# Kernel tuning notes

Measured on AMD Instinct MI355X. Metric: run time of the kernel, lower is better.

The kernel has to match this reference:

```python
import jax, jax.numpy as jnp
import numpy as np

N_NODES = 20000
N_EDGES = 320000
N_GRAPHS = 200
N_LAYERS = 2
TOWERS = 5
F_IN = 75        # divide_input=False -> each tower sees the full 75-dim input
F_OUT = 15       # out_channels // towers = 75 // 5
EDGE_DIM = 50
POST_IN = (4 * 3 + 1) * F_IN  # 4 aggregators * 3 scalers + self = 975
EPS_STD = 1e-5
EPS_BN = 1e-5


def setup_inputs() -> dict:
    key = jax.random.key(0)
    ks = jax.random.split(key, 16)
    x_idx = jax.random.randint(ks[0], (N_NODES,), 0, 10000)
    edge_index = jax.random.randint(ks[1], (2, N_EDGES), 0, N_NODES)
    edge_attr_idx = jax.random.randint(ks[2], (N_EDGES,), 0, 100)
    batch_idx = jnp.sort(jax.random.randint(ks[3], (N_NODES,), 0, N_GRAPHS))

    def g(k, shp, fan):
        return jax.random.normal(k, shp, jnp.float32) * np.float32(1.0 / np.sqrt(fan))

    inp = dict(
        x_idx=x_idx, edge_index=edge_index, edge_attr_idx=edge_attr_idx, batch_idx=batch_idx,
        node_emb=g(ks[4], (10000, F_IN), 1.0),
        edge_emb=g(ks[5], (100, EDGE_DIM), 1.0),
        W_edge=g(ks[6], (N_LAYERS, EDGE_DIM, F_IN), EDGE_DIM),
        b_edge=jnp.zeros((N_LAYERS, F_IN), jnp.float32),
        W_pre=g(ks[7], (N_LAYERS, TOWERS, 3 * F_IN, F_IN), 3 * F_IN),
        b_pre=jnp.zeros((N_LAYERS, TOWERS, F_IN), jnp.float32),
        W_post=g(ks[8], (N_LAYERS, TOWERS, POST_IN, F_OUT), POST_IN),
        b_post=jnp.zeros((N_LAYERS, TOWERS, F_OUT), jnp.float32),
        W_lin=g(ks[9], (N_LAYERS, F_IN, F_IN), F_IN),
        b_lin=jnp.zeros((N_LAYERS, F_IN), jnp.float32),
        bn_gamma=jnp.ones((N_LAYERS, F_IN), jnp.float32),
        bn_beta=jnp.zeros((N_LAYERS, F_IN), jnp.float32),
        W1=g(ks[10], (75, 50), 75), b1=jnp.zeros((50,), jnp.float32),
        W2=g(ks[11], (50, 25), 50), b2=jnp.zeros((25,), jnp.float32),
        W3=g(ks[12], (25, 1), 25), b3=jnp.zeros((1,), jnp.float32),
    )
    return inp


def reference(x_idx, edge_index, edge_attr_idx, batch_idx,
              node_emb, edge_emb, W_edge, b_edge, W_pre, b_pre,
              W_post, b_post, W_lin, b_lin, bn_gamma, bn_beta,
              W1, b1, W2, b2, W3, b3):
    src, dst = edge_index[0], edge_index[1]  # flow source_to_target: aggregate at dst
    x = node_emb[x_idx]                      # [N, 75]
    e_raw = edge_emb[edge_attr_idx]          # [E, 50]

    # in-degree based scalers (PNA); avg log-degree from this graph's degree histogram
    deg = jax.ops.segment_sum(jnp.ones((N_EDGES,), jnp.float32), dst, num_segments=N_NODES)
    avg_log = jnp.mean(jnp.log(deg + 1.0))
    deg_c = jnp.maximum(deg, 1.0)
    amp = (jnp.log(deg_c + 1.0) / avg_log)[:, None, None]
    att = (avg_log / jnp.log(deg_c + 1.0))[:, None, None]
    has_in = (deg > 0.0)[:, None, None]
    inv_deg = (1.0 / deg_c)[:, None, None]

    for l in range(N_LAYERS):
        # edge encoder (shared across towers)
        e = e_raw @ W_edge[l] + b_edge[l]                            # [E, 75]
        # message: since divide_input=False all towers see the same concat input
        h = jnp.concatenate([x[dst], x[src], e], axis=-1)            # [E, 225]
        m = jnp.einsum('ec,tcf->etf', h, W_pre[l]) + b_pre[l]        # [E, T, 75]
        # multi-aggregator reduction at dst
        mean = jax.ops.segment_sum(m, dst, num_segments=N_NODES) * inv_deg
        mean_sq = jax.ops.segment_sum(m * m, dst, num_segments=N_NODES) * inv_deg
        std = jnp.sqrt(jax.nn.relu(mean_sq - mean * mean) + EPS_STD)
        mn = jnp.where(has_in, jax.ops.segment_min(m, dst, num_segments=N_NODES), 0.0)
        mx = jnp.where(has_in, jax.ops.segment_max(m, dst, num_segments=N_NODES), 0.0)
        aggr = jnp.concatenate([mean, mn, mx, std], axis=-1)         # [N, T, 300]
        # degree scalers: identity, amplification, attenuation
        out = jnp.concatenate([aggr, aggr * amp, aggr * att], axis=-1)  # [N, T, 900]
        # update: concat self features, per-tower post MLP, then shared lin
        xt = jnp.broadcast_to(x[:, None, :], (N_NODES, TOWERS, F_IN))
        h2 = jnp.concatenate([xt, out], axis=-1)                     # [N, T, 975]
        y = jnp.einsum('ntc,tcf->ntf', h2, W_post[l]) + b_post[l]    # [N, T, 15]
        y = y.reshape(N_NODES, TOWERS * F_OUT) @ W_lin[l] + b_lin[l] # [N, 75]
        # BatchNorm (training-mode batch stats, biased variance) + ReLU
        mu = jnp.mean(y, axis=0)
        var = jnp.mean((y - mu) ** 2, axis=0)
        y = (y - mu) * jax.lax.rsqrt(var + EPS_BN) * bn_gamma[l] + bn_beta[l]
        x = jax.nn.relu(y)

    pooled = jax.ops.segment_sum(x, batch_idx, num_segments=N_GRAPHS)  # [G, 75]
    h = jax.nn.relu(pooled @ W1 + b1)
    h = jax.nn.relu(h @ W2 + b2)
    return h @ W3 + b3                                               # [G, 1]
```

## Files before the change

kernel.cpp:

```cpp
#include <hip/hip_runtime.h>
#include <hip/hip_bf16.h>
#include <math.h>

#define NN 20000
#define NE 320000
#define NG 200
#define FI 75
#define NT 5
#define FO 15
#define CH 375
#define PI 975

typedef __attribute__((ext_vector_type(8))) short v8s;
typedef __attribute__((ext_vector_type(4))) float v4f;

__device__ __forceinline__ unsigned short f2bfu(float v) {
  __hip_bfloat16 h = __float2bfloat16(v);
  return *reinterpret_cast<unsigned short*>(&h);
}
__device__ __forceinline__ float uif(unsigned u) { return __uint_as_float(u); }

__global__ __launch_bounds__(256) void k_mega1(
    const int* __restrict__ xidx, const float* __restrict__ emb, float* __restrict__ x,
    const int* __restrict__ dstp, int* __restrict__ deg,
    const float* __restrict__ eemb, const float* __restrict__ W_edge,
    const float* __restrict__ b_edge, float* __restrict__ te,
    const float* __restrict__ W_pre, float* __restrict__ WAs,
    const float* __restrict__ W_post, float* __restrict__ V,
    const float* __restrict__ b_post, const float* __restrict__ W_lin,
    const float* __restrict__ b_lin, float* __restrict__ bc) {
  __shared__ float S[FI * 16];
  int b = blockIdx.x, tid = threadIdx.x;
  if (b < 5860) {
    int i = b * 256 + tid;
    if (i < NN * FI) {
      int n = i / FI, f = i - n * FI;
      x[i] = emb[xidx[n] * FI + f];
    }
  } else if (b < 7110) {
    int e = (b - 5860) * 256 + tid;
    if (e < NE) atomicAdd(&deg[dstp[e]], 1);
  } else if (b < 7310) {
    int la = b - 7110;
    int l = la / 100, a = la - l * 100;
    int f = tid;
    if (f < FI) {
      float acc = b_edge[l * FI + f];
      for (int j = 0; j < 50; ++j)
        acc = fmaf(eemb[a * 50 + j], W_edge[(l * 50 + j) * FI + f], acc);
      te[la * FI + f] = acc;
    }
  } else if (b < 7530) {
    int i = (b - 7310) * 256 + tid;
    if (i < 2 * FI * CH) {
      int c = i % CH;
      int k = (i / CH) % FI;
      int l = i / (CH * FI);
      int t = c / FI, f = c - t * FI;
      WAs[i] = W_pre[((size_t)(l * NT + t) * 225 + FI + k) * FI + f];
    }
  } else if (b < 7560) {
    int bid = b - 7530;
    int g = bid % 3;
    int lt = bid / 3;
    for (int idx = tid; idx < FI * 16; idx += 256) {
      int q = idx >> 4, f = idx & 15;
      float v = 0.f;
      if (f < FO) {
        const float* wb = W_post + (size_t)lt * PI * FO;
        int rowb = FI + g * 300 + q;
        v = wb[rowb * FO + f] + wb[(rowb + FI) * FO + f] + wb[(rowb + 2 * FI) * FO + f];
      }
      S[idx] = v;
    }
    __syncthreads();
    for (int idx = tid; idx < FI * 16; idx += 256) {
      int j = idx >> 4, f = idx & 15;
      float acc = 0.f;
      const float* wr = W_pre + ((size_t)lt * 225 + j) * FI;
      for (int q = 0; q < FI; ++q) acc = fmaf(wr[q], S[q * 16 + f], acc);
      V[((size_t)bid * FI + j) * 16 + f] = acc;
    }
  } else {
    int l = b - 7560;
    int g = tid;
    if (g < FI) {
      float acc = b_lin[l * FI + g];
      for (int j = 0; j < FI; ++j)
        acc = fmaf(b_post[l * FI + j], W_lin[(l * FI + j) * FI + g], acc);
      bc[l * 76 + g] = acc;
    }
  }
}

__global__ __launch_bounds__(1024) void k_mega2(
    const int* __restrict__ deg, int* __restrict__ off, int* __restrict__ cur,
    float* __restrict__ avglog,
    const float* __restrict__ te, const float* __restrict__ W_pre,
    const float* __restrict__ b_pre, unsigned short* __restrict__ tm,
    const float* __restrict__ W_post, const float* __restrict__ V,
    unsigned short* __restrict__ Bp,
    const float* __restrict__ WAs, unsigned short* __restrict__ Bxs) {
  __shared__ float red[1024];
  int b = blockIdx.x, t = threadIdx.x;
  if (b == 0) {
    int* wsum = (int*)red;
    int base = t * 20;
    int loc[20];
    int s = 0;
#pragma unroll
    for (int j = 0; j < 20; ++j) {
      int i = base + j;
      int v = (i < NN) ? deg[i] : 0;
      loc[j] = s;
      s += v;
    }
    int lane = t & 63, w = t >> 6;
    int inc = s;
    for (int o = 1; o < 64; o <<= 1) {
      int u = __shfl_up(inc, o, 64);
      if (lane >= o) inc += u;
    }
    if (lane == 63) wsum[w] = inc;
    __syncthreads();
    if (t == 0) {
      int a = 0;
#pragma unroll
      for (int k = 0; k < 16; ++k) { int v = wsum[k]; wsum[k] = a; a += v; }
    }
    __syncthreads();
    int tex = wsum[w] + inc - s;
#pragma unroll
    for (int j = 0; j < 20; ++j) {
      int i = base + j;
      if (i < NN) { int e = tex + loc[j]; off[i] = e; cur[i] = e; }
    }
    if (t == 1023) off[NN] = tex + s;
  } else if (b == 1) {
    float s = 0.f;
    for (int i = t; i < NN; i += 1024) s += logf((float)deg[i] + 1.f);
    red[t] = s;
    __syncthreads();
    for (int o = 512; o > 0; o >>= 1) {
      if (t < o) red[t] += red[t + o];
      __syncthreads();
    }
    if (t == 0) avglog[0] = red[0] / (float)NN;
  } else if (b < 77) {
    int idx = (b - 2) * 1024 + t;
    if (idx < 76800) {
      int la = idx / 384, c = idx - la * 384;
      int l = la / 100;
      float acc = 0.f;
      if (c < CH) {
        int tt = c / FI, f = c - tt * FI;
        acc = b_pre[(l * NT + tt) * FI + f];
        const float* ter = te + la * FI;
        for (int k = 0; k < FI; ++k)
          acc = fmaf(ter[k], W_pre[((size_t)(l * NT + tt) * 225 + 150 + k) * FI + f], acc);
      }
      tm[(size_t)la * 384 + c] = f2bfu(acc);
    }
  } else if (b < 302) {
    int i = (b - 77) * 1024 + t;
    if (i < 230400) {
      int j = i & 7;
      int lane = (i >> 3) & 63;
      int rem = i >> 9;
      int kb = rem % 15; rem /= 15;
      int g = rem % 3; rem /= 3;
      int tt = rem % 5;
      int l = rem / 5;
      int k = kb * 32 + (lane >> 4) * 8 + j;
      int f = lane & 15;
      float w = 0.f;
      if (f < FO) {
        int lt = l * NT + tt;
        if (k < 300) {
          int a = k / 75, ch = k - a * 75;
          w = W_post[((size_t)lt * PI + FI + g * 300 + a * 75 + ch) * FO + f];
        } else if (k >= 320 && k < 395) {
          w = V[(((size_t)(lt * 3 + g)) * FI + (k - 320)) * 16 + f];
        } else if (k >= 395 && k < 470 && g == 0) {
          w = W_post[((size_t)lt * PI + (k - 395)) * FO + f];
        }
      }
      Bp[i] = f2bfu(w);
    }
  } else {
    int i = (b - 302) * 1024 + t;
    if (i < 73728) {
      int j = i & 7;
      int lane = (i >> 3) & 63;
      int rem = i >> 9;
      int nt = rem % 24; rem /= 24;
      int kb = rem % 3;
      int l = rem / 3;
      int k = kb * 32 + (lane >> 4) * 8 + j;
      int n = nt * 16 + (lane & 15);
      float w = 0.f;
      if (k < FI && n < CH) w = WAs[(size_t)l * FI * CH + k * CH + n];
      Bxs[i] = f2bfu(w);
    }
  }
}

__global__ __launch_bounds__(256) void k_mega3(
    const int* __restrict__ srcp, const int* __restrict__ dstp,
    const int* __restrict__ attr, int* __restrict__ cur, int2* __restrict__ csr,
    const int* __restrict__ deg, const float* __restrict__ avglog,
    float* __restrict__ amp, float* __restrict__ att, float* __restrict__ inv) {
  int b = blockIdx.x, t = threadIdx.x;
  if (b < 1250) {
    int e = b * 256 + t;
    if (e < NE) {
      int pos = atomicAdd(&cur[dstp[e]], 1);
      csr[pos] = make_int2(srcp[e], attr[e]);
    }
  } else {
    int i = (b - 1250) * 256 + t;
    if (i < NN) {
      float dc = fmaxf((float)deg[i], 1.f);
      float ld = logf(dc + 1.f);
      float av = avglog[0];
      amp[i] = ld / av;
      att[i] = av / ld;
      inv[i] = 1.f / dc;
    }
  }
}

__global__ __launch_bounds__(256) void k_gemm_xs(const float* __restrict__ x,
                                                 const unsigned short* __restrict__ BxsL,
                                                 unsigned short* __restrict__ xsb,
                                                 const int* __restrict__ deg,
                                                 unsigned short* __restrict__ xh,
                                                 float* __restrict__ bnsum) {
  int tid = threadIdx.x;
  if (blockIdx.y == 1) {
    if (blockIdx.x == 0 && tid < 150) bnsum[tid] = 0.f;
    for (int i = blockIdx.x * 256 + tid; i < NN * 160; i += 625 * 256) {
      int r = i / 160, k = i - r * 160;
      float v = 0.f;
      if (k < FI) v = x[(size_t)r * FI + k] * ((deg[r] > 0) ? 1.f : 0.f);
      else if (k < 150) v = x[(size_t)r * FI + k - FI];
      xh[i] = f2bfu(v);
    }
    return;
  }
  __shared__ unsigned short As[32 * 104];
  __shared__ unsigned short Os[32 * 384];
  int m0 = blockIdx.x * 32;
  for (int i = tid; i < 32 * 104; i += 256) {
    int r = i / 104, k = i - r * 104;
    As[i] = (k < FI) ? f2bfu(x[(size_t)(m0 + r) * FI + k]) : 0;
  }
  __syncthreads();
  int lane = tid & 63, w = tid >> 6;
  int m16 = lane & 15, quad = lane >> 4;
  v4f acc0[6], acc1[6];
#pragma unroll
  for (int nt = 0; nt < 6; ++nt) {
    acc0[nt] = {0.f, 0.f, 0.f, 0.f};
    acc1[nt] = {0.f, 0.f, 0.f, 0.f};
  }
  const unsigned short* arow0 = As + m16 * 104 + quad * 8;
  const unsigned short* arow1 = As + (16 + m16) * 104 + quad * 8;
#pragma unroll
  for (int kb = 0; kb < 3; ++kb) {
    v8s a0 = *(const v8s*)(arow0 + kb * 32);
    v8s a1 = *(const v8s*)(arow1 + kb * 32);
#pragma unroll
    for (int nt = 0; nt < 6; ++nt) {
      v8s bf = *(const v8s*)(BxsL + ((size_t)(kb * 24 + w * 6 + nt) * 64 + lane) * 8);
      acc0[nt] = __builtin_amdgcn_mfma_f32_16x16x32_bf16(a0, bf, acc0[nt], 0, 0, 0);
      acc1[nt] = __builtin_amdgcn_mfma_f32_16x16x32_bf16(a1, bf, acc1[nt], 0, 0, 0);
    }
  }
#pragma unroll
  for (int nt = 0; nt < 6; ++nt) {
    int col = w * 96 + nt * 16 + m16;
#pragma unroll
    for (int r = 0; r < 4; ++r) {
      Os[(quad * 4 + r) * 384 + col] = f2bfu(acc0[nt][r]);
      Os[(16 + quad * 4 + r) * 384 + col] = f2bfu(acc1[nt][r]);
    }
  }
  __syncthreads();
  uint4* dst = (uint4*)(xsb + (size_t)m0 * 384);
  const uint4* src = (const uint4*)Os;
  for (int i = tid; i < 1536; i += 256) dst[i] = src[i];
}

__global__ __launch_bounds__(192) void k_aggregate(int n0, int cn,
    const unsigned short* __restrict__ xs, const int2* __restrict__ csr,
    const int* __restrict__ off, const float* __restrict__ inv_deg,
    const unsigned short* __restrict__ tm, unsigned short* __restrict__ aggA) {
  __shared__ unsigned short sm[4 * 1600];
  int tid = threadIdx.x;
  int sub = tid / 48;
  int lane48 = tid - sub * 48;
  int rel0 = blockIdx.x * 4;
  int rel = rel0 + sub;
  for (int idx = tid; idx < 400; idx += 192) {
    int h = idx / 100, pp = idx - h * 100;
    int t = pp / 20, cc = pp - t * 20;
    sm[h * 1600 + t * 320 + 300 + cc] = 0;
  }
  if (rel < cn) {
    int n = n0 + rel;
    int c0 = lane48 * 8;
    int o0 = off[n], o1 = off[n + 1];
    float s[8], q[8], mn[8], mx[8];
#pragma unroll
    for (int j = 0; j < 8; ++j) {
      s[j] = 0.f; q[j] = 0.f; mn[j] = INFINITY; mx[j] = -INFINITY;
    }
    auto proc = [&](uint4 xv, uint4 tv) {
      unsigned xa[4] = {xv.x, xv.y, xv.z, xv.w};
      unsigned ta[4] = {tv.x, tv.y, tv.z, tv.w};
#pragma unroll
      for (int j = 0; j < 4; ++j) {
        float z0 = uif(xa[j] << 16) + uif(ta[j] << 16);
        float z1 = uif(xa[j] & 0xffff0000u) + uif(ta[j] & 0xffff0000u);
        s[2 * j] += z0; q[2 * j] = fmaf(z0, z0, q[2 * j]);
        mn[2 * j] = fminf(mn[2 * j], z0); mx[2 * j] = fmaxf(mx[2 * j], z0);
        s[2 * j + 1] += z1; q[2 * j + 1] = fmaf(z1, z1, q[2 * j + 1]);
        mn[2 * j + 1] = fminf(mn[2 * j + 1], z1); mx[2 * j + 1] = fmaxf(mx[2 * j + 1], z1);
      }
    };
    int i = o0;
    for (; i + 8 <= o1; i += 8) {
      int2 e0 = csr[i], e1 = csr[i + 1], e2 = csr[i + 2], e3 = csr[i + 3];
      int2 e4 = csr[i + 4], e5 = csr[i + 5], e6 = csr[i + 6], e7 = csr[i + 7];
      uint4 x0 = *(const uint4*)(xs + (size_t)e0.x * 384 + c0);
      uint4 t0 = *(const uint4*)(tm + (size_t)e0.y * 384 + c0);
      uint4 x1 = *(const uint4*)(xs + (size_t)e1.x * 384 + c0);
      uint4 t1 = *(const uint4*)(tm + (size_t)e1.y * 384 + c0);
      uint4 x2 = *(const uint4*)(xs + (size_t)e2.x * 384 + c0);
      uint4 t2 = *(const uint4*)(tm + (size_t)e2.y * 384 + c0);
      uint4 x3 = *(const uint4*)(xs + (size_t)e3.x * 384 + c0);
      uint4 t3 = *(const uint4*)(tm + (size_t)e3.y * 384 + c0);
      uint4 x4 = *(const uint4*)(xs + (size_t)e4.x * 384 + c0);
      uint4 t4 = *(const uint4*)(tm + (size_t)e4.y * 384 + c0);
      uint4 x5 = *(const uint4*)(xs + (size_t)e5.x * 384 + c0);
      uint4 t5 = *(const uint4*)(tm + (size_t)e5.y * 384 + c0);
      uint4 x6 = *(const uint4*)(xs + (size_t)e6.x * 384 + c0);
      uint4 t6 = *(const uint4*)(tm + (size_t)e6.y * 384 + c0);
      uint4 x7 = *(const uint4*)(xs + (size_t)e7.x * 384 + c0);
      uint4 t7 = *(const uint4*)(tm + (size_t)e7.y * 384 + c0);
      proc(x0, t0); proc(x1, t1); proc(x2, t2); proc(x3, t3);
      proc(x4, t4); proc(x5, t5); proc(x6, t6); proc(x7, t7);
    }
    for (; i + 2 <= o1; i += 2) {
      int2 e0 = csr[i], e1 = csr[i + 1];
      uint4 x0 = *(const uint4*)(xs + (size_t)e0.x * 384 + c0);
      uint4 t0 = *(const uint4*)(tm + (size_t)e0.y * 384 + c0);
      uint4 x1 = *(const uint4*)(xs + (size_t)e1.x * 384 + c0);
      uint4 t1 = *(const uint4*)(tm + (size_t)e1.y * 384 + c0);
      proc(x0, t0); proc(x1, t1);
    }
    if (i < o1) {
      int2 e0 = csr[i];
      uint4 x0 = *(const uint4*)(xs + (size_t)e0.x * 384 + c0);
      uint4 t0 = *(const uint4*)(tm + (size_t)e0.y * 384 + c0);
      proc(x0, t0);
    }
    float inv = inv_deg[n];
    bool empty = (o1 == o0);
    unsigned short* srow = sm + sub * 1600;
#pragma unroll
    for (int j = 0; j < 8; ++j) {
      int c = c0 + j;
      if (c < CH) {
        float me = s[j] * inv;
        float sd = sqrtf(fmaxf(q[j] * inv - me * me, 0.f) + 1e-5f);
        float mnv = empty ? 0.f : mn[j];
        float mxv = empty ? 0.f : mx[j];
        int t = c / 75, ch = c - t * 75;
        unsigned short* bb = srow + t * 320;
        bb[ch] = f2bfu(me);
        bb[75 + ch] = f2bfu(mnv);
        bb[150 + ch] = f2bfu(mxv);
        bb[225 + ch] = f2bfu(sd);
      }
    }
  }
  __syncthreads();
  int nrow = cn - rel0;
  if (nrow > 4) nrow = 4;
  if (nrow > 0) {
    int nu4 = nrow * 200;
    uint4* dst = (uint4*)(aggA + (size_t)rel0 * 1600);
    const uint4* src = (const uint4*)sm;
    for (int idx = tid; idx < nu4; idx += 192) dst[idx] = src[idx];
  }
}

__global__ __launch_bounds__(128) void k_post2(int n0, int nend,
    const unsigned short* __restrict__ aggA, const unsigned short* __restrict__ xh,
    const unsigned short* __restrict__ Bp, const float* __restrict__ amp,
    const float* __restrict__ att, const float* __restrict__ Wl,
    const float* __restrict__ bcL, float* __restrict__ yout,
    float* __restrict__ bnsum) {
  __shared__ float zs[32][76];
  __shared__ float Ws[FI * 76];
  __shared__ float ysum[FI], ysq[FI];
  int tid = threadIdx.x;
  for (int i = tid; i < FI * FI; i += 128) {
    int k = i / FI, f = i - k * FI;
    Ws[k * 76 + f] = Wl[i];
  }
  if (tid < FI) { ysum[tid] = 0.f; ysq[tid] = 0.f; }
  int lane = tid & 63, wv = tid >> 6;
  int m16 = lane & 15, quad = lane >> 4;
  int relA = blockIdx.x * 32 + wv * 16 + m16;
  const unsigned short* arow = aggA + (size_t)relA * 1600 + quad * 8;
  const unsigned short* xrow = xh + (size_t)(n0 + relA) * 160 + quad * 8;
  for (int t = 0; t < NT; ++t) {
    const unsigned short* bp = Bp + ((size_t)t * 3 * 15 * 64) * 8 + lane * 8;
    v4f a0 = {0.f, 0.f, 0.f, 0.f}, a1 = a0, a2 = a0;
#pragma unroll
    for (int kb = 0; kb < 15; ++kb) {
      v8s av = *(const v8s*)((kb < 10) ? (arow + t * 320 + kb * 32)
                                       : (xrow + (kb - 10) * 32));
      const unsigned short* bb = bp + (size_t)kb * 512;
      v8s b0 = *(const v8s*)(bb);
      v8s b1 = *(const v8s*)(bb + 15 * 512);
      v8s b2 = *(const v8s*)(bb + 30 * 512);
      a0 = __builtin_amdgcn_mfma_f32_16x16x32_bf16(av, b0, a0, 0, 0, 0);
      a1 = __builtin_amdgcn_mfma_f32_16x16x32_bf16(av, b1, a1, 0, 0, 0);
      a2 = __builtin_amdgcn_mfma_f32_16x16x32_bf16(av, b2, a2, 0, 0, 0);
    }
    int f = m16;
    if (f < FO) {
      int relD0 = wv * 16 + quad * 4;
#pragma unroll
      for (int r = 0; r < 4; ++r) {
        int nd = n0 + blockIdx.x * 32 + relD0 + r;
        if (nd < nend) {
          float zz = a0[r] + amp[nd] * a1[r] + att[nd] * a2[r];
          zs[relD0 + r][t * FO + f] = zz;
        }
      }
    }
  }
  __syncthreads();
  int nl = tid >> 2, fg = tid & 3;
  int f0 = fg * 19;
  int n = n0 + blockIdx.x * 32 + nl;
  if (n < nend) {
    float acc[19];
#pragma unroll
    for (int i = 0; i < 19; ++i) acc[i] = bcL[f0 + i];
    for (int k = 0; k < FI; ++k) {
      float a = zs[nl][k];
#pragma unroll
      for (int i = 0; i < 19; ++i) acc[i] = fmaf(a, Ws[k * 76 + f0 + i], acc[i]);
    }
#pragma unroll
    for (int i = 0; i < 19; ++i) {
      int f = f0 + i;
      if (f < FI) {
        float v = acc[i];
        yout[(size_t)n * FI + f] = v;
        atomicAdd(&ysum[f], v);
        atomicAdd(&ysq[f], v * v);
      }
    }
  }
  __syncthreads();
  if (tid < FI) {
    atomicAdd(&bnsum[tid], ysum[tid]);
    atomicAdd(&bnsum[FI + tid], ysq[tid]);
  }
}

__global__ __launch_bounds__(256) void k_bnfinapply(const float* __restrict__ y,
    const float* __restrict__ bnsum, const float* __restrict__ gamL,
    const float* __restrict__ betL, float* __restrict__ xo,
    const int* __restrict__ batch, float* __restrict__ pooled, int dopool) {
  __shared__ float sc[150];
  int tid = threadIdx.x;
  if (tid < FI) {
    float mu = bnsum[tid] / (float)NN;
    float var = bnsum[FI + tid] / (float)NN - mu * mu;
    float scl = gamL[tid] * rsqrtf(var + 1e-5f);
    sc[tid] = scl;
    sc[FI + tid] = betL[tid] - mu * scl;
  }
  if (!dopool) {
    for (int i = blockIdx.x * 256 + tid; i < NG * FI; i += gridDim.x * 256)
      pooled[i] = 0.f;
  }
  __syncthreads();
  int stride = gridDim.x * 256;
  for (int i = blockIdx.x * 256 + tid; i < NN * FI; i += stride) {
    int n = i / FI, f = i - n * FI;
    float v = fmaxf(fmaf(y[i], sc[f], sc[FI + f]), 0.f);
    xo[i] = v;
    if (dopool) atomicAdd(&pooled[batch[n] * FI + f], v);
  }
}

__global__ void k_head(const float* __restrict__ pooled, const float* __restrict__ W1,
                       const float* __restrict__ b1, const float* __restrict__ W2,
                       const float* __restrict__ b2, const float* __restrict__ W3,
                       const float* __restrict__ b3, float* __restrict__ out) {
  __shared__ float p[FI], h1[50], h2[25];
  int g = blockIdx.x, t = threadIdx.x;
  for (int i = t; i < FI; i += 64) p[i] = pooled[g * FI + i];
  __syncthreads();
  if (t < 50) {
    float a = b1[t];
    for (int j = 0; j < FI; ++j) a = fmaf(p[j], W1[j * 50 + t], a);
    h1[t] = fmaxf(a, 0.f);
  }
  __syncthreads();
  if (t < 25) {
    float a = b2[t];
    for (int j = 0; j < 50; ++j) a = fmaf(h1[j], W2[j * 25 + t], a);
    h2[t] = fmaxf(a, 0.f);
  }
  __syncthreads();
  if (t == 0) {
    float a = b3[0];
    for (int j = 0; j < 25; ++j) a = fmaf(h2[j], W3[j], a);
    out[g] = a;
  }
}

extern "C" void kernel_launch(void* const* d_in, const int* in_sizes, int n_in,
                              void* d_out, int out_size, void* d_ws, size_t ws_size,
                              hipStream_t stream) {
  const int* x_idx = (const int*)d_in[0];
  const int* eidx  = (const int*)d_in[1];
  const int* srcp  = eidx;
  const int* dstp  = eidx + NE;
  const int* eattr = (const int*)d_in[2];
  const int* batch = (const int*)d_in[3];
  const float* node_emb = (const float*)d_in[4];
  const float* edge_emb = (const float*)d_in[5];
  const float* W_edge = (const float*)d_in[6];
  const float* b_edge = (const float*)d_in[7];
  const float* W_pre  = (const float*)d_in[8];
  const float* b_pre  = (const float*)d_in[9];
  const float* W_post = (const float*)d_in[10];
  const float* b_post = (const float*)d_in[11];
  const float* W_lin  = (const float*)d_in[12];
  const float* b_lin  = (const float*)d_in[13];
  const float* gam = (const float*)d_in[14];
  const float* bet = (const float*)d_in[15];
  const float* W1 = (const float*)d_in[16];
  const float* b1 = (const float*)d_in[17];
  const float* W2 = (const float*)d_in[18];
  const float* b2 = (const float*)d_in[19];
  const float* W3 = (const float*)d_in[20];
  const float* b3 = (const float*)d_in[21];

  char* p = (char*)d_ws;
  auto alloc = [&](size_t b) -> char* {
    char* r = p;
    p += (b + 255) & ~(size_t)255;
    return r;
  };
  float* x_a   = (float*)alloc((size_t)NN * FI * 4);
  float* x_b   = (float*)alloc((size_t)NN * FI * 4);
  unsigned short* xs_bf = (unsigned short*)alloc((size_t)NN * 384 * 2);
  float* z     = (float*)alloc((size_t)NN * FI * 4);
  unsigned short* xh = (unsigned short*)alloc((size_t)(NN + 32) * 160 * 2);
  float* te    = (float*)alloc(2 * 100 * FI * 4);
  unsigned short* tm_bf = (unsigned short*)alloc((size_t)2 * 100 * 384 * 2);
  float* WAs   = (float*)alloc((size_t)2 * FI * CH * 4);
  float* V     = (float*)alloc((size_t)2 * NT * 3 * FI * 16 * 4);
  unsigned short* Bpk = (unsigned short*)alloc((size_t)230400 * 2);
  unsigned short* Bxs = (unsigned short*)alloc((size_t)73728 * 2);
  float* bc    = (float*)alloc(2 * 76 * 4);
  float* ampv  = (float*)alloc((size_t)NN * 4);
  float* attv  = (float*)alloc((size_t)NN * 4);
  float* invv  = (float*)alloc((size_t)NN * 4);
  float* avglog = (float*)alloc(256);
  float* bnsum = (float*)alloc(2 * FI * 4);
  float* pooled = (float*)alloc((size_t)NG * FI * 4);
  int* deg = (int*)alloc((size_t)NN * 4);
  int* off = (int*)alloc((size_t)(NN + 1) * 4);
  int* cur = (int*)alloc((size_t)NN * 4);
  int2* csr = (int2*)alloc((size_t)NE * 8);
  size_t used = (size_t)(p - (char*)d_ws);
  int chunkN = NN;
  while (chunkN > 2500 &&
         used + (size_t)((chunkN + 31) & ~31) * 1600 * 2 + (1 << 20) > ws_size)
    chunkN >>= 1;
  int rows = (chunkN + 31) & ~31;
  unsigned short* aggA = (unsigned short*)alloc((size_t)rows * 1600 * 2);

  hipMemsetAsync(deg, 0, (size_t)NN * 4, stream);

  k_mega1<<<7562, 256, 0, stream>>>(x_idx, node_emb, x_a, dstp, deg,
                                    edge_emb, W_edge, b_edge, te,
                                    W_pre, WAs, W_post, V,
                                    b_post, W_lin, b_lin, bc);
  k_mega2<<<374, 1024, 0, stream>>>(deg, off, cur, avglog,
                                    te, W_pre, b_pre, tm_bf, W_post, V, Bpk,
                                    WAs, Bxs);
  k_mega3<<<1329, 256, 0, stream>>>(srcp, dstp, eattr, cur, csr,
                                    deg, avglog, ampv, attv, invv);

  for (int l = 0; l < 2; ++l) {
    const float* xin = (l == 0) ? x_a : x_b;
    float* xout = (l == 0) ? x_b : x_a;
    k_gemm_xs<<<dim3(625, 2), 256, 0, stream>>>(xin, Bxs + (size_t)l * 36864,
                                                xs_bf, deg, xh, bnsum);
    for (int n0 = 0; n0 < NN; n0 += chunkN) {
      int cn = (NN - n0 < chunkN) ? (NN - n0) : chunkN;
      k_aggregate<<<(cn + 3) / 4, 192, 0, stream>>>(n0, cn, xs_bf, csr, off, invv,
                                                    tm_bf + (size_t)l * 100 * 384, aggA);
      k_post2<<<(cn + 31) / 32, 128, 0, stream>>>(
          n0, n0 + cn, aggA, xh, Bpk + (size_t)l * 115200, ampv, attv,
          W_lin + (size_t)l * FI * FI, bc + l * 76, z, bnsum);
    }
    k_bnfinapply<<<1250, 256, 0, stream>>>(z, bnsum, gam + l * FI, bet + l * FI,
                                           xout, batch, pooled, (l == 1) ? 1 : 0);
  }

  k_head<<<NG, 64, 0, stream>>>(pooled, W1, b1, W2, b2, W3, b3, (float*)d_out);
}
```

Before: 471.9 us.

## Use bf16 MFMA for the W_lin projection in k_post2 with 64-row blocks

The scalar FP32 W_lin projection in k_post2 becomes bf16 MFMA tiles. W_lin is prepacked into MFMA layout in extra k_mega2 blocks, and the intermediate z is kept as bf16 in shared memory. Blocks grow to 256 threads covering 64 nodes, which removes the per-block shared-memory load of W_lin and the per-thread 19-wide FMA loop. The cost is that z is rounded to bf16 before the linear layer, and the aggA/xh padding plus node clamping change to fit 64-row tiles.

After: 465.2 us. About the same (-1.4%).

```diff
diff --git a/kernel.cpp b/kernel.cpp
--- a/kernel.cpp
+++ b/kernel.cpp
@@ -100,7 +100,8 @@
     const float* __restrict__ b_pre, unsigned short* __restrict__ tm,
     const float* __restrict__ W_post, const float* __restrict__ V,
     unsigned short* __restrict__ Bp,
-    const float* __restrict__ WAs, unsigned short* __restrict__ Bxs) {
+    const float* __restrict__ WAs, unsigned short* __restrict__ Bxs,
+    const float* __restrict__ W_lin, unsigned short* __restrict__ Blin) {
   __shared__ float red[1024];
   int b = blockIdx.x, t = threadIdx.x;
   if (b == 0) {
@@ -187,7 +188,7 @@
       }
       Bp[i] = f2bfu(w);
     }
-  } else {
+  } else if (b < 374) {
     int i = (b - 302) * 1024 + t;
     if (i < 73728) {
       int j = i & 7;
@@ -201,6 +202,21 @@
       float w = 0.f;
       if (k < FI && n < CH) w = WAs[(size_t)l * FI * CH + k * CH + n];
       Bxs[i] = f2bfu(w);
+    }
+  } else {
+    int i = (b - 374) * 1024 + t;
+    if (i < 15360) {
+      int j = i & 7;
+      int lane = (i >> 3) & 63;
+      int rem = i >> 9;
+      int nt = rem % 5; rem /= 5;
+      int kb = rem % 3;
+      int l = rem / 3;
+      int k = kb * 32 + (lane >> 4) * 8 + j;
+      int f = nt * 16 + (lane & 15);
+      float w = 0.f;
+      if (k < FI && f < FI) w = W_lin[(size_t)l * FI * FI + k * FI + f];
+      Blin[i] = f2bfu(w);
     }
   }
 }
@@ -397,24 +413,23 @@
   }
 }
 
-__global__ __launch_bounds__(128) void k_post2(int n0, int nend,
+__global__ __launch_bounds__(256) void k_post2(int n0, int nend,
     const unsigned short* __restrict__ aggA, const unsigned short* __restrict__ xh,
     const unsigned short* __restrict__ Bp, const float* __restrict__ amp,
-    const float* __restrict__ att, const float* __restrict__ Wl,
+    const float* __restrict__ att, const unsigned short* __restrict__ BlinL,
     const float* __restrict__ bcL, float* __restrict__ yout,
     float* __restrict__ bnsum) {
-  __shared__ float zs[32][76];
-  __shared__ float Ws[FI * 76];
+  __shared__ unsigned short zs[64 * 96];
   __shared__ float ysum[FI], ysq[FI];
   int tid = threadIdx.x;
-  for (int i = tid; i < FI * FI; i += 128) {
-    int k = i / FI, f = i - k * FI;
-    Ws[k * 76 + f] = Wl[i];
-  }
   if (tid < FI) { ysum[tid] = 0.f; ysq[tid] = 0.f; }
+  for (int i = tid; i < 64 * 21; i += 256) {
+    int r = i / 21, k = 75 + i - r * 21;
+    zs[r * 96 + k] = 0;
+  }
   int lane = tid & 63, wv = tid >> 6;
   int m16 = lane & 15, quad = lane >> 4;
-  int relA = blockIdx.x * 32 + wv * 16 + m16;
+  int relA = blockIdx.x * 64 + wv * 16 + m16;
   const unsigned short* arow = aggA + (size_t)relA * 1600 + quad * 8;
   const unsigned short* xrow = xh + (size_t)(n0 + relA) * 160 + quad * 8;
   for (int t = 0; t < NT; ++t) {
@@ -434,38 +449,45 @@
     }
     int f = m16;
     if (f < FO) {
-      int relD0 = wv * 16 + quad * 4;
+      int relZ = wv * 16 + quad * 4;
 #pragma unroll
       for (int r = 0; r < 4; ++r) {
-        int nd = n0 + blockIdx.x * 32 + relD0 + r;
-        if (nd < nend) {
-          float zz = a0[r] + amp[nd] * a1[r] + att[nd] * a2[r];
-          zs[relD0 + r][t * FO + f] = zz;
+        int nd = n0 + blockIdx.x * 64 + relZ + r;
+        int ndc = (nd < NN) ? nd : (NN - 1);
+        float zz = a0[r] + amp[ndc] * a1[r] + att[ndc] * a2[r];
+        zs[(relZ + r) * 96 + t * FO + f] = f2bfu(zz);
+      }
+    }
+  }
+  __syncthreads();
+  const unsigned short* zrow = zs + (wv * 16 + m16) * 96 + quad * 8;
+  v4f acc2[5];
+#pragma unroll
+  for (int nt = 0; nt < 5; ++nt) acc2[nt] = {0.f, 0.f, 0.f, 0.f};
+#pragma unroll
+  for (int kb = 0; kb < 3; ++kb) {
+    v8s av = *(const v8s*)(zrow + kb * 32);
+#pragma unroll
+    for (int nt = 0; nt < 5; ++nt) {
+      v8s bl = *(const v8s*)(BlinL + ((size_t)(kb * 5 + nt) * 64 + lane) * 8);
+      acc2[nt] = __builtin_amdgcn_mfma_f32_16x16x32_bf16(av, bl, acc2[nt], 0, 0, 0);
+    }
+  }
+  int nb = n0 + blockIdx.x * 64 + wv * 16 + quad * 4;
+#pragma unroll
+  for (int nt = 0; nt < 5; ++nt) {
+    int f = nt * 16 + m16;
+    if (f < FI) {
+      float bcf = bcL[f];
+#pragma unroll
+      for (int r = 0; r < 4; ++r) {
+        int n = nb + r;
+        if (n < nend) {
+          float v = acc2[nt][r] + bcf;
+          yout[(size_t)n * FI + f] = v;
+          atomicAdd(&ysum[f], v);
+          atomicAdd(&ysq[f], v * v);
         }
-      }
-    }
-  }
-  __syncthreads();
-  int nl = tid >> 2, fg = tid & 3;
-  int f0 = fg * 19;
-  int n = n0 + blockIdx.x * 32 + nl;
-  if (n < nend) {
-    float acc[19];
-#pragma unroll
-    for (int i = 0; i < 19; ++i) acc[i] = bcL[f0 + i];
-    for (int k = 0; k < FI; ++k) {
-      float a = zs[nl][k];
-#pragma unroll
-      for (int i = 0; i < 19; ++i) acc[i] = fmaf(a, Ws[k * 76 + f0 + i], acc[i]);
-    }
-#pragma unroll
-    for (int i = 0; i < 19; ++i) {
-      int f = f0 + i;
-      if (f < FI) {
-        float v = acc[i];
-        yout[(size_t)n * FI + f] = v;
-        atomicAdd(&ysum[f], v);
-        atomicAdd(&ysq[f], v * v);
       }
     }
   }
@@ -568,13 +590,14 @@
   float* x_b   = (float*)alloc((size_t)NN * FI * 4);
   unsigned short* xs_bf = (unsigned short*)alloc((size_t)NN * 384 * 2);
   float* z     = (float*)alloc((size_t)NN * FI * 4);
-  unsigned short* xh = (unsigned short*)alloc((size_t)(NN + 32) * 160 * 2);
+  unsigned short* xh = (unsigned short*)alloc((size_t)(NN + 64) * 160 * 2);
   float* te    = (float*)alloc(2 * 100 * FI * 4);
   unsigned short* tm_bf = (unsigned short*)alloc((size_t)2 * 100 * 384 * 2);
   float* WAs   = (float*)alloc((size_t)2 * FI * CH * 4);
   float* V     = (float*)alloc((size_t)2 * NT * 3 * FI * 16 * 4);
   unsigned short* Bpk = (unsigned short*)alloc((size_t)230400 * 2);
   unsigned short* Bxs = (unsigned short*)alloc((size_t)73728 * 2);
+  unsigned short* Blin = (unsigned short*)alloc((size_t)15360 * 2);
   float* bc    = (float*)alloc(2 * 76 * 4);
   float* ampv  = (float*)alloc((size_t)NN * 4);
   float* attv  = (float*)alloc((size_t)NN * 4);
@@ -589,9 +612,9 @@
   size_t used = (size_t)(p - (char*)d_ws);
   int chunkN = NN;
   while (chunkN > 2500 &&
-         used + (size_t)((chunkN + 31) & ~31) * 1600 * 2 + (1 << 20) > ws_size)
+         used + (size_t)((chunkN + 63) & ~63) * 1600 * 2 + (1 << 20) > ws_size)
     chunkN >>= 1;
-  int rows = (chunkN + 31) & ~31;
+  int rows = (chunkN + 63) & ~63;
   unsigned short* aggA = (unsigned short*)alloc((size_t)rows * 1600 * 2);
 
   hipMemsetAsync(deg, 0, (size_t)NN * 4, stream);
@@ -600,9 +623,9 @@
                                     edge_emb, W_edge, b_edge, te,
                                     W_pre, WAs, W_post, V,
                                     b_post, W_lin, b_lin, bc);
-  k_mega2<<<374, 1024, 0, stream>>>(deg, off, cur, avglog,
+  k_mega2<<<389, 1024, 0, stream>>>(deg, off, cur, avglog,
                                     te, W_pre, b_pre, tm_bf, W_post, V, Bpk,
-                                    WAs, Bxs);
+                                    WAs, Bxs, W_lin, Blin);
   k_mega3<<<1329, 256, 0, stream>>>(srcp, dstp, eattr, cur, csr,
                                     deg, avglog, ampv, attv, invv);
 
@@ -615,9 +638,9 @@
       int cn = (NN - n0 < chunkN) ? (NN - n0) : chunkN;
       k_aggregate<<<(cn + 3) / 4, 192, 0, stream>>>(n0, cn, xs_bf, csr, off, invv,
                                                     tm_bf + (size_t)l * 100 * 384, aggA);
-      k_post2<<<(cn + 31) / 32, 128, 0, stream>>>(
+      k_post2<<<(cn + 63) / 64, 256, 0, stream>>>(
           n0, n0 + cn, aggA, xh, Bpk + (size_t)l * 115200, ampv, attv,
-          W_lin + (size_t)l * FI * FI, bc + l * 76, z, bnsum);
+          Blin + (size_t)l * 7680, bc + l * 76, z, bnsum);
     }
     k_bnfinapply<<<1250, 256, 0, stream>>>(z, bnsum, gam + l * FI, bet + l * FI,
                                            xout, batch, pooled, (l == 1) ? 1 : 0);
```
